# Performance work log

Measured on AMD Instinct MI355X. Metric: run time of the kernel, lower is better.

Reference implementation:

```python
import jax, jax.numpy as jnp
import numpy as np

B, L, N, D, C = 256, 512, 64, 32, 100  # batch, latent_dim, num_concepts, box_dim, num_classes


def setup_inputs() -> dict:
    key = jax.random.key(0)
    ks = jax.random.split(key, 11)
    s = 0.02  # weight init scale
    return {
        "h": jax.random.normal(ks[0], (B, L), dtype=jnp.float32),
        "Wc": jax.random.normal(ks[1], (N, L, D), dtype=jnp.float32) * s,
        "bc": jax.random.normal(ks[2], (N, D), dtype=jnp.float32) * s,
        "Wo": jax.random.normal(ks[3], (N, L, D), dtype=jnp.float32) * s,
        "bo": jax.random.normal(ks[4], (N, D), dtype=jnp.float32) * s,
        "Wp": jax.random.normal(ks[5], (N, 2 * D), dtype=jnp.float32) * s,
        "bp": jax.random.normal(ks[6], (N,), dtype=jnp.float32) * s,
        "W1": jax.random.normal(ks[7], (N * 2 * D, C), dtype=jnp.float32) * s,
        "b1": jax.random.normal(ks[8], (C,), dtype=jnp.float32) * s,
        "W2": jax.random.normal(ks[9], (N * N, C), dtype=jnp.float32) * s,
        "b2": jax.random.normal(ks[10], (C,), dtype=jnp.float32) * s,
    }


def reference(h, Wc, bc, Wo, bo, Wp, bp, W1, b1, W2, b2):
    EPS = 1e-6
    batch = h.shape[0]
    # Batched per-concept projections (replaces N un-batched Linears)
    x_m = jnp.einsum('bl,nld->bnd', h, Wc) + bc                    # [B,N,D] centers
    delta = jax.nn.softplus(jnp.einsum('bl,nld->bnd', h, Wo) + bo)  # [B,N,D] offsets
    box = jnp.concatenate([x_m, delta], axis=-1)                    # [B,N,2D]
    # Per-concept probability heads
    p_hat = jax.nn.sigmoid(jnp.einsum('bnd,nd->bn', box, Wp) + bp)  # [B,N]
    # Pairwise intersection volumes, fully broadcast (replaces N^2 loop)
    lo = x_m - delta  # [B,N,D]
    hi = x_m + delta
    inter = jnp.minimum(hi[:, :, None, :], hi[:, None, :, :]) - \
            jnp.maximum(lo[:, :, None, :], lo[:, None, :, :])       # [B,N,N,D]
    inter_off = jax.nn.relu(inter) * 0.5
    vol_inter = jnp.prod(inter_off + EPS, axis=-1)                  # [B,N,N]
    vol = jnp.prod(delta + EPS, axis=-1)                            # [B,N]
    V = vol_inter / vol[:, None, :]                                 # V[b,i,j] = |i∩j|/|j|
    # Classification heads
    aligned_flat = (box * p_hat[..., None]).reshape(batch, -1)      # [B, N*2D]
    y_hat = aligned_flat @ W1 + b1 + V.reshape(batch, -1) @ W2 + b2  # [B,C]
    return y_hat, p_hat, V
```

## Files before the change

kernel.cpp:

```cpp
#include <hip/hip_runtime.h>
#include <hip/hip_bf16.h>
#include <cstdint>

constexpr int Bb = 256, Ll = 512, Nn = 64, Dd = 32, Cc = 100;
constexpr float EPS = 1e-6f;

typedef __attribute__((ext_vector_type(8))) short short8;
typedef __attribute__((ext_vector_type(4))) float f32x4;

__device__ __forceinline__ unsigned short f2bf(float f) {
  union { float f; uint32_t u; } v; v.f = f;
  uint32_t r = v.u + 0x7FFFu + ((v.u >> 16) & 1u);
  return (unsigned short)(r >> 16);
}

__global__ __launch_bounds__(256) void kA(
    const float* __restrict__ h,
    const float* __restrict__ Wc,
    const float* __restrict__ bc,
    const float* __restrict__ Wo,
    const float* __restrict__ bo,
    const float* __restrict__ Wp,
    const float* __restrict__ bp,
    const float* __restrict__ b1,
    const float* __restrict__ b2,
    float* __restrict__ xm_ws,
    float* __restrict__ dl_ws,
    float* __restrict__ ph_ws,
    float* __restrict__ out_ph,
    float* __restrict__ out_y)
{
  const int n  = blockIdx.x;
  const int bt = blockIdx.y * 64;
  const int t  = threadIdx.x;
  const int w  = t >> 6, l = t & 63;
  const int lr = l & 15, lg = l >> 4;

  {
    const int bid = blockIdx.x + Nn * blockIdx.y;
    if (t < Cc) out_y[bid * Cc + t] = b1[t] + b2[t];
  }

  __shared__ unsigned short hb[64][72];
  __shared__ unsigned short wbT[64][72];

  f32x4 acc[4] = {};

  const int hr = t >> 2,       hc  = (t & 3) * 16;
  const int wk = (t >> 3) * 2, wcq = (t & 7) * 4;
  const float* hsrc  = h  + (bt + hr) * Ll + hc;
  const float* wcsrc = Wc + n * (Ll * Dd) + wk * Dd + wcq;
  const float* wosrc = Wo + n * (Ll * Dd) + wk * Dd + wcq;

  float4 hp0, hp1, hp2, hp3, c0, c1, o0, o1;
  auto fetch = [&](int k0) {
    const float* hs = hsrc + k0;
    hp0 = *(const float4*)(hs);
    hp1 = *(const float4*)(hs + 4);
    hp2 = *(const float4*)(hs + 8);
    hp3 = *(const float4*)(hs + 12);
    const float* ws = wcsrc + k0 * Dd;
    c0 = *(const float4*)(ws);
    c1 = *(const float4*)(ws + Dd);
    const float* os = wosrc + k0 * Dd;
    o0 = *(const float4*)(os);
    o1 = *(const float4*)(os + Dd);
  };

  fetch(0);
  for (int ch = 0; ch < 8; ch++) {
    __syncthreads();
    {
      unsigned short* hd = &hb[hr][hc];
      hd[0]  = f2bf(hp0.x); hd[1]  = f2bf(hp0.y);
      hd[2]  = f2bf(hp0.z); hd[3]  = f2bf(hp0.w);
      hd[4]  = f2bf(hp1.x); hd[5]  = f2bf(hp1.y);
      hd[6]  = f2bf(hp1.z); hd[7]  = f2bf(hp1.w);
      hd[8]  = f2bf(hp2.x); hd[9]  = f2bf(hp2.y);
      hd[10] = f2bf(hp2.z); hd[11] = f2bf(hp2.w);
      hd[12] = f2bf(hp3.x); hd[13] = f2bf(hp3.y);
      hd[14] = f2bf(hp3.z); hd[15] = f2bf(hp3.w);
    }
    {
      const float* c0p = &c0.x; const float* c1p = &c1.x;
      const float* o0p = &o0.x; const float* o1p = &o1.x;
      #pragma unroll
      for (int i = 0; i < 4; i++) {
        unsigned int pc = (unsigned int)f2bf(c0p[i]) |
                          ((unsigned int)f2bf(c1p[i]) << 16);
        *(unsigned int*)&wbT[wcq + i][wk] = pc;
        unsigned int po = (unsigned int)f2bf(o0p[i]) |
                          ((unsigned int)f2bf(o1p[i]) << 16);
        *(unsigned int*)&wbT[32 + wcq + i][wk] = po;
      }
    }
    __syncthreads();
    if (ch < 7) fetch((ch + 1) * 64);
    const int arow = w * 16 + lr;
    #pragma unroll
    for (int ks = 0; ks < 2; ks++) {
      const int ko = ks * 32 + lg * 8;
      const short8 av = *(const short8*)&hb[arow][ko];
      #pragma unroll
      for (int nf = 0; nf < 4; nf++) {
        const short8 bv = *(const short8*)&wbT[nf * 16 + lr][ko];
        acc[nf] = __builtin_amdgcn_mfma_f32_16x16x32_bf16(av, bv, acc[nf],
                                                          0, 0, 0);
      }
    }
  }

  const float bc0 = bc[n * Dd + lr],      bc1 = bc[n * Dd + 16 + lr];
  const float bo0 = bo[n * Dd + lr],      bo1 = bo[n * Dd + 16 + lr];
  const float wp0 = Wp[n * 64 + lr],      wp1 = Wp[n * 64 + 16 + lr];
  const float wp2 = Wp[n * 64 + 32 + lr], wp3 = Wp[n * 64 + 48 + lr];
  const float bpv = bp[n];

  #pragma unroll
  for (int q = 0; q < 4; q++) {
    const int b = bt + w * 16 + lg * 4 + q;
    const float xm0  = acc[0][q] + bc0;
    const float xm1  = acc[1][q] + bc1;
    const float pre0 = acc[2][q] + bo0;
    const float pre1 = acc[3][q] + bo1;
    const float dl0 = fmaxf(pre0, 0.f) + log1pf(expf(-fabsf(pre0)));
    const float dl1 = fmaxf(pre1, 0.f) + log1pf(expf(-fabsf(pre1)));
    float* xp = xm_ws + b * 2048 + n * Dd;
    float* dp = dl_ws + b * 2048 + n * Dd;
    xp[lr] = xm0;  xp[16 + lr] = xm1;
    dp[lr] = dl0;  dp[16 + lr] = dl1;
    float pp = xm0 * wp0 + xm1 * wp1 + dl0 * wp2 + dl1 * wp3;
    pp += __shfl_xor(pp, 1);
    pp += __shfl_xor(pp, 2);
    pp += __shfl_xor(pp, 4);
    pp += __shfl_xor(pp, 8);
    if (lr == 0) {
      const float ph = 1.f / (1.f + expf(-(pp + bpv)));
      ph_ws[b * 64 + n] = ph;
      out_ph[b * 64 + n] = ph;
    }
  }
}

__global__ __launch_bounds__(512) void kB(
    const float* __restrict__ xm_ws,
    const float* __restrict__ dl_ws,
    float* __restrict__ out_V)
{
  const int b = blockIdx.x, t = threadIdx.x;
  __shared__ float lo[64][36];
  __shared__ float hi[64][36];
  __shared__ float rvol[64];

  {
    const int n = t >> 3, dd = (t & 7) * 4;
    float4 x = *(const float4*)(xm_ws + b * 2048 + n * Dd + dd);
    float4 g = *(const float4*)(dl_ws + b * 2048 + n * Dd + dd);
    lo[n][dd + 0] = x.x - g.x;  hi[n][dd + 0] = x.x + g.x;
    lo[n][dd + 1] = x.y - g.y;  hi[n][dd + 1] = x.y + g.y;
    lo[n][dd + 2] = x.z - g.z;  hi[n][dd + 2] = x.z + g.z;
    lo[n][dd + 3] = x.w - g.w;  hi[n][dd + 3] = x.w + g.w;
  }
  if (t < 64) {
    const float* dp = dl_ws + b * 2048 + t * Dd;
    float p = 1.f;
    #pragma unroll
    for (int dd = 0; dd < 32; dd++) p *= dp[dd] + EPS;
    rvol[t] = 1.f / p;
  }
  __syncthreads();

  const int i0 = t >> 6;
  const int j  = t & 63;
  #pragma unroll 1
  for (int it = 0; it < 8; it++) {
    const int i = i0 + 8 * it;
    float prod = 1.f;
    #pragma unroll
    for (int dd = 0; dd < 32; dd += 4) {
      float4 hj = *(const float4*)&hi[j][dd];
      float4 lj = *(const float4*)&lo[j][dd];
      float4 hv = *(const float4*)&hi[i][dd];
      float4 lv = *(const float4*)&lo[i][dd];
      float v0 = fmaxf(fminf(hv.x, hj.x) - fmaxf(lv.x, lj.x), 0.f) * 0.5f + EPS;
      float v1 = fmaxf(fminf(hv.y, hj.y) - fmaxf(lv.y, lj.y), 0.f) * 0.5f + EPS;
      float v2 = fmaxf(fminf(hv.z, hj.z) - fmaxf(lv.z, lj.z), 0.f) * 0.5f + EPS;
      float v3 = fmaxf(fminf(hv.w, hj.w) - fmaxf(lv.w, lj.w), 0.f) * 0.5f + EPS;
      prod *= v0 * v1 * v2 * v3;
    }
    out_V[b * 4096 + i * 64 + j] = prod * rvol[j];
  }
}

__global__ __launch_bounds__(256) void kC(
    const float* __restrict__ xm_ws,
    const float* __restrict__ dl_ws,
    const float* __restrict__ ph_ws,
    const float* __restrict__ Vb,
    const float* __restrict__ W1,
    const float* __restrict__ W2,
    float* __restrict__ out_y)
{
  const int Mg = blockIdx.x;
  const int s  = blockIdx.y;
  const bool isV = (s >= 32);
  const int m0 = (s & 31) * 128;
  const float* __restrict__ W = isV ? W2 : W1;
  const int b0 = Mg * 64;

  __shared__ unsigned short Ab[64][40];
  __shared__ unsigned short Wb[112][40];

  const int t = threadIdx.x;
  const int w = t >> 6, l = t & 63;
  const int lr = l & 15, lg = l >> 4;

  f32x4 acc[7] = {};

  const int ar = t >> 2, ak8 = (t & 3) * 8;
  const int arow = b0 + ar;
  const int wc = t & 127, wkb = t >> 7;

  float4 a0, a1;
  float wv[16];

  auto fetch = [&](int ch) {
    const int kb = m0 + ch * 32;
    const int mk = kb + ak8;
    if (!isV) {
      const int nn = mk >> 6, sub = mk & 63;
      const float phv = ph_ws[arow * 64 + nn];
      const float* src = (sub < 32)
          ? (xm_ws + arow * 2048 + nn * Dd + sub)
          : (dl_ws + arow * 2048 + nn * Dd + (sub - 32));
      a0 = *(const float4*)(src);
      a1 = *(const float4*)(src + 4);
      a0.x *= phv; a0.y *= phv; a0.z *= phv; a0.w *= phv;
      a1.x *= phv; a1.y *= phv; a1.z *= phv; a1.w *= phv;
    } else {
      const float* src = Vb + arow * 4096 + mk;
      a0 = *(const float4*)(src);
      a1 = *(const float4*)(src + 4);
    }
    if (wc < Cc) {
      #pragma unroll
      for (int i = 0; i < 16; i++)
        wv[i] = W[(kb + wkb + 2 * i) * Cc + wc];
    }
  };

  fetch(0);
  for (int ch = 0; ch < 4; ch++) {
    __syncthreads();
    {
      unsigned short* ad = &Ab[ar][ak8];
      ad[0] = f2bf(a0.x); ad[1] = f2bf(a0.y);
      ad[2] = f2bf(a0.z); ad[3] = f2bf(a0.w);
      ad[4] = f2bf(a1.x); ad[5] = f2bf(a1.y);
      ad[6] = f2bf(a1.z); ad[7] = f2bf(a1.w);
    }
    if (wc < Cc) {
      #pragma unroll
      for (int i = 0; i < 16; i++)
        Wb[wc][wkb + 2 * i] = f2bf(wv[i]);
    } else if (wc < 112) {
      #pragma unroll
      for (int i = 0; i < 16; i++)
        Wb[wc][wkb + 2 * i] = 0;
    }
    __syncthreads();
    if (ch < 3) fetch(ch + 1);
    const short8 av = *(const short8*)&Ab[w * 16 + lr][lg * 8];
    #pragma unroll
    for (int nf = 0; nf < 7; nf++) {
      const short8 bv = *(const short8*)&Wb[nf * 16 + lr][lg * 8];
      acc[nf] = __builtin_amdgcn_mfma_f32_16x16x32_bf16(av, bv, acc[nf],
                                                        0, 0, 0);
    }
  }

  #pragma unroll
  for (int nf = 0; nf < 7; nf++) {
    const int col = nf * 16 + lr;
    if (col < Cc) {
      #pragma unroll
      for (int q = 0; q < 4; q++) {
        const int row = b0 + w * 16 + lg * 4 + q;
        atomicAdd(out_y + row * Cc + col, acc[nf][q]);
      }
    }
  }
}

extern "C" void kernel_launch(void* const* d_in, const int* in_sizes, int n_in,
                              void* d_out, int out_size, void* d_ws, size_t ws_size,
                              hipStream_t stream) {
  const float* h  = (const float*)d_in[0];
  const float* Wc = (const float*)d_in[1];
  const float* bc = (const float*)d_in[2];
  const float* Wo = (const float*)d_in[3];
  const float* bo = (const float*)d_in[4];
  const float* Wp = (const float*)d_in[5];
  const float* bp = (const float*)d_in[6];
  const float* W1 = (const float*)d_in[7];
  const float* b1 = (const float*)d_in[8];
  const float* W2 = (const float*)d_in[9];
  const float* b2 = (const float*)d_in[10];

  float* out    = (float*)d_out;
  float* out_y  = out;
  float* out_ph = out + Bb * Cc;
  float* out_V  = out + Bb * Cc + Bb * Nn;

  float* xm = (float*)d_ws;
  float* dl = xm + Bb * Nn * Dd;
  float* ph = dl + Bb * Nn * Dd;

  kA<<<dim3(Nn, Bb / 64), 256, 0, stream>>>(h, Wc, bc, Wo, bo, Wp, bp,
                                            b1, b2, xm, dl, ph, out_ph, out_y);
  kB<<<Bb, 512, 0, stream>>>(xm, dl, out_V);
  kC<<<dim3(4, 64), 256, 0, stream>>>(xm, dl, ph, (const float*)out_V,
                                      W1, W2, out_y);
}
```

Baseline: 48.96 us.

## Pre-pack bf16 A operand in producers and double K-chunk in GEMM kernel

kA now writes the p_hat-scaled box features as bf16 into a packed activation buffer, and kB writes a bf16 copy of V alongside the fp32 output. The classification GEMM kernel then reads ready-made bf16 rows with vector loads, dropping the fp32 gather, scaling and conversion. It also processes 64-wide K chunks (two chunks instead of four), which means fewer barriers. kB keeps the j-row lo/hi in registers and computes the j volume per thread instead of in a separate 64-thread pass. The cost is extra global writes in kA and kB and more registers from the larger weight prefetch (32 floats).

After: 48.64 us. About the same (-0.7%).

```diff
diff --git a/kernel.cpp b/kernel.cpp
--- a/kernel.cpp
+++ b/kernel.cpp
@@ -26,7 +26,7 @@
     const float* __restrict__ b2,
     float* __restrict__ xm_ws,
     float* __restrict__ dl_ws,
-    float* __restrict__ ph_ws,
+    unsigned short* __restrict__ abuf,
     float* __restrict__ out_ph,
     float* __restrict__ out_y)
 {
@@ -134,23 +134,25 @@
     pp += __shfl_xor(pp, 2);
     pp += __shfl_xor(pp, 4);
     pp += __shfl_xor(pp, 8);
-    if (lr == 0) {
-      const float ph = 1.f / (1.f + expf(-(pp + bpv)));
-      ph_ws[b * 64 + n] = ph;
-      out_ph[b * 64 + n] = ph;
-    }
+    const float ph = 1.f / (1.f + expf(-(pp + bpv)));
+    unsigned short* ab = abuf + b * 8192 + n * 64;
+    ab[lr]      = f2bf(xm0 * ph);
+    ab[16 + lr] = f2bf(xm1 * ph);
+    ab[32 + lr] = f2bf(dl0 * ph);
+    ab[48 + lr] = f2bf(dl1 * ph);
+    if (lr == 0) out_ph[b * 64 + n] = ph;
   }
 }
 
 __global__ __launch_bounds__(512) void kB(
     const float* __restrict__ xm_ws,
     const float* __restrict__ dl_ws,
-    float* __restrict__ out_V)
+    float* __restrict__ out_V,
+    unsigned short* __restrict__ abuf)
 {
   const int b = blockIdx.x, t = threadIdx.x;
   __shared__ float lo[64][36];
   __shared__ float hi[64][36];
-  __shared__ float rvol[64];
 
   {
     const int n = t >> 3, dd = (t & 7) * 4;
@@ -161,42 +163,49 @@
     lo[n][dd + 2] = x.z - g.z;  hi[n][dd + 2] = x.z + g.z;
     lo[n][dd + 3] = x.w - g.w;  hi[n][dd + 3] = x.w + g.w;
   }
-  if (t < 64) {
-    const float* dp = dl_ws + b * 2048 + t * Dd;
-    float p = 1.f;
-    #pragma unroll
-    for (int dd = 0; dd < 32; dd++) p *= dp[dd] + EPS;
-    rvol[t] = 1.f / p;
-  }
   __syncthreads();
 
-  const int i0 = t >> 6;
   const int j  = t & 63;
+  const int wv = t >> 6;
+
+  float4 lj[8], hj[8];
+  #pragma unroll
+  for (int q = 0; q < 8; q++) {
+    lj[q] = *(const float4*)&lo[j][q * 4];
+    hj[q] = *(const float4*)&hi[j][q * 4];
+  }
+  float pr = 1.f;
+  #pragma unroll
+  for (int q = 0; q < 8; q++) {
+    pr *= ((hj[q].x - lj[q].x) * 0.5f + EPS);
+    pr *= ((hj[q].y - lj[q].y) * 0.5f + EPS);
+    pr *= ((hj[q].z - lj[q].z) * 0.5f + EPS);
+    pr *= ((hj[q].w - lj[q].w) * 0.5f + EPS);
+  }
+  const float rv = 1.f / pr;
+
   #pragma unroll 1
   for (int it = 0; it < 8; it++) {
-    const int i = i0 + 8 * it;
+    const int i = wv * 8 + it;
     float prod = 1.f;
     #pragma unroll
-    for (int dd = 0; dd < 32; dd += 4) {
-      float4 hj = *(const float4*)&hi[j][dd];
-      float4 lj = *(const float4*)&lo[j][dd];
-      float4 hv = *(const float4*)&hi[i][dd];
-      float4 lv = *(const float4*)&lo[i][dd];
-      float v0 = fmaxf(fminf(hv.x, hj.x) - fmaxf(lv.x, lj.x), 0.f) * 0.5f + EPS;
-      float v1 = fmaxf(fminf(hv.y, hj.y) - fmaxf(lv.y, lj.y), 0.f) * 0.5f + EPS;
-      float v2 = fmaxf(fminf(hv.z, hj.z) - fmaxf(lv.z, lj.z), 0.f) * 0.5f + EPS;
-      float v3 = fmaxf(fminf(hv.w, hj.w) - fmaxf(lv.w, lj.w), 0.f) * 0.5f + EPS;
+    for (int q = 0; q < 8; q++) {
+      const float4 hv = *(const float4*)&hi[i][q * 4];
+      const float4 lv = *(const float4*)&lo[i][q * 4];
+      float v0 = fmaxf((fminf(hv.x, hj[q].x) - fmaxf(lv.x, lj[q].x)) * 0.5f + EPS, EPS);
+      float v1 = fmaxf((fminf(hv.y, hj[q].y) - fmaxf(lv.y, lj[q].y)) * 0.5f + EPS, EPS);
+      float v2 = fmaxf((fminf(hv.z, hj[q].z) - fmaxf(lv.z, lj[q].z)) * 0.5f + EPS, EPS);
+      float v3 = fmaxf((fminf(hv.w, hj[q].w) - fmaxf(lv.w, lj[q].w)) * 0.5f + EPS, EPS);
       prod *= v0 * v1 * v2 * v3;
     }
-    out_V[b * 4096 + i * 64 + j] = prod * rvol[j];
+    const float V = prod * rv;
+    out_V[b * 4096 + i * 64 + j] = V;
+    abuf[b * 8192 + 4096 + i * 64 + j] = f2bf(V);
   }
 }
 
 __global__ __launch_bounds__(256) void kC(
-    const float* __restrict__ xm_ws,
-    const float* __restrict__ dl_ws,
-    const float* __restrict__ ph_ws,
-    const float* __restrict__ Vb,
+    const unsigned short* __restrict__ abuf,
     const float* __restrict__ W1,
     const float* __restrict__ W2,
     float* __restrict__ out_y)
@@ -208,8 +217,8 @@
   const float* __restrict__ W = isV ? W2 : W1;
   const int b0 = Mg * 64;
 
-  __shared__ unsigned short Ab[64][40];
-  __shared__ unsigned short Wb[112][40];
+  __shared__ unsigned short Ab[64][76];
+  __shared__ unsigned short Wb[112][76];
 
   const int t = threadIdx.x;
   const int w = t >> 6, l = t & 63;
@@ -217,65 +226,50 @@
 
   f32x4 acc[7] = {};
 
-  const int ar = t >> 2, ak8 = (t & 3) * 8;
-  const int arow = b0 + ar;
+  const int ar = t >> 2, ak = (t & 3) * 16;
+  const unsigned short* asrc =
+      abuf + (b0 + ar) * 8192 + (isV ? 4096 : 0) + m0 + ak;
   const int wc = t & 127, wkb = t >> 7;
 
-  float4 a0, a1;
-  float wv[16];
+  short8 a0, a1;
+  float wv[32];
 
   auto fetch = [&](int ch) {
-    const int kb = m0 + ch * 32;
-    const int mk = kb + ak8;
-    if (!isV) {
-      const int nn = mk >> 6, sub = mk & 63;
-      const float phv = ph_ws[arow * 64 + nn];
-      const float* src = (sub < 32)
-          ? (xm_ws + arow * 2048 + nn * Dd + sub)
-          : (dl_ws + arow * 2048 + nn * Dd + (sub - 32));
-      a0 = *(const float4*)(src);
-      a1 = *(const float4*)(src + 4);
-      a0.x *= phv; a0.y *= phv; a0.z *= phv; a0.w *= phv;
-      a1.x *= phv; a1.y *= phv; a1.z *= phv; a1.w *= phv;
-    } else {
-      const float* src = Vb + arow * 4096 + mk;
-      a0 = *(const float4*)(src);
-      a1 = *(const float4*)(src + 4);
-    }
+    const int kb = ch * 64;
+    a0 = *(const short8*)(asrc + kb);
+    a1 = *(const short8*)(asrc + kb + 8);
     if (wc < Cc) {
-      #pragma unroll
-      for (int i = 0; i < 16; i++)
-        wv[i] = W[(kb + wkb + 2 * i) * Cc + wc];
+      const float* wp = W + (m0 + kb + wkb) * Cc + wc;
+      #pragma unroll
+      for (int i = 0; i < 32; i++) wv[i] = wp[2 * i * Cc];
     }
   };
 
   fetch(0);
-  for (int ch = 0; ch < 4; ch++) {
+  #pragma unroll
+  for (int ch = 0; ch < 2; ch++) {
     __syncthreads();
-    {
-      unsigned short* ad = &Ab[ar][ak8];
-      ad[0] = f2bf(a0.x); ad[1] = f2bf(a0.y);
-      ad[2] = f2bf(a0.z); ad[3] = f2bf(a0.w);
-      ad[4] = f2bf(a1.x); ad[5] = f2bf(a1.y);
-      ad[6] = f2bf(a1.z); ad[7] = f2bf(a1.w);
-    }
+    *(short8*)&Ab[ar][ak]     = a0;
+    *(short8*)&Ab[ar][ak + 8] = a1;
     if (wc < Cc) {
       #pragma unroll
-      for (int i = 0; i < 16; i++)
-        Wb[wc][wkb + 2 * i] = f2bf(wv[i]);
+      for (int i = 0; i < 32; i++) Wb[wc][wkb + 2 * i] = f2bf(wv[i]);
     } else if (wc < 112) {
       #pragma unroll
-      for (int i = 0; i < 16; i++)
-        Wb[wc][wkb + 2 * i] = 0;
+      for (int i = 0; i < 32; i++) Wb[wc][wkb + 2 * i] = 0;
     }
     __syncthreads();
-    if (ch < 3) fetch(ch + 1);
-    const short8 av = *(const short8*)&Ab[w * 16 + lr][lg * 8];
+    if (ch == 0) fetch(1);
     #pragma unroll
-    for (int nf = 0; nf < 7; nf++) {
-      const short8 bv = *(const short8*)&Wb[nf * 16 + lr][lg * 8];
-      acc[nf] = __builtin_amdgcn_mfma_f32_16x16x32_bf16(av, bv, acc[nf],
-                                                        0, 0, 0);
+    for (int ks = 0; ks < 2; ks++) {
+      const int ko = ks * 32 + lg * 8;
+      const short8 av = *(const short8*)&Ab[w * 16 + lr][ko];
+      #pragma unroll
+      for (int nf = 0; nf < 7; nf++) {
+        const short8 bv = *(const short8*)&Wb[nf * 16 + lr][ko];
+        acc[nf] = __builtin_amdgcn_mfma_f32_16x16x32_bf16(av, bv, acc[nf],
+                                                          0, 0, 0);
+      }
     }
   }
 
@@ -314,11 +308,10 @@
 
   float* xm = (float*)d_ws;
   float* dl = xm + Bb * Nn * Dd;
-  float* ph = dl + Bb * Nn * Dd;
+  unsigned short* abuf = (unsigned short*)(dl + Bb * Nn * Dd);
 
   kA<<<dim3(Nn, Bb / 64), 256, 0, stream>>>(h, Wc, bc, Wo, bo, Wp, bp,
-                                            b1, b2, xm, dl, ph, out_ph, out_y);
-  kB<<<Bb, 512, 0, stream>>>(xm, dl, out_V);
-  kC<<<dim3(4, 64), 256, 0, stream>>>(xm, dl, ph, (const float*)out_V,
-                                      W1, W2, out_y);
-}
+                                            b1, b2, xm, dl, abuf, out_ph, out_y);
+  kB<<<Bb, 512, 0, stream>>>(xm, dl, out_V, abuf);
+  kC<<<dim3(4, 64), 256, 0, stream>>>(abuf, W1, W2, out_y);
+}
```
